# Kernel tuning notes

Measured on AMD Instinct MI355X. Metric: run time of the kernel, lower is better.

## Reference

```python
import jax, jax.numpy as jnp
import numpy as np

NEG_SLOPE = 0.2


def gat_conv(x, W, att_s, att_d, bias, src, dst, heads, out_c, concat):
    n = x.shape[0]
    h = (x @ W).reshape(n, heads, out_c)                      # [N,H,C]
    a_s = (h * att_s).sum(-1)                                 # [N,H]
    a_d = (h * att_d).sum(-1)                                 # [N,H]
    logits = jax.nn.leaky_relu(a_s[src] + a_d[dst], NEG_SLOPE)  # [E,H]
    # segment softmax over incoming edges of each dst node (per head)
    m = jax.ops.segment_max(logits, dst, num_segments=n)
    e = jnp.exp(logits - m[dst])
    denom = jax.ops.segment_sum(e, dst, num_segments=n)
    alpha = e / denom[dst]                                    # [E,H]
    msg = h[src] * alpha[:, :, None]                          # [E,H,C]
    out = jax.ops.segment_sum(msg, dst, num_segments=n)       # [N,H,C]
    out = out.reshape(n, heads * out_c) if concat else out.mean(axis=1)
    return out + bias


def setup_inputs() -> dict:
    key = jax.random.key(0)
    ks = jax.random.split(key, 9)
    N, IN, OUT, E = 100000, 256, 40, 1600000
    return {
        "x": jax.random.normal(ks[0], (N, IN), jnp.float32),
        "edge_index": jax.random.randint(ks[1], (2, E), 0, N, jnp.int32),
        "W1": jax.random.normal(ks[2], (IN, 64), jnp.float32) * (1.0 / np.sqrt(IN)),
        "att_src1": jax.random.normal(ks[3], (8, 8), jnp.float32) * 0.1,
        "att_dst1": jax.random.normal(ks[4], (8, 8), jnp.float32) * 0.1,
        "b1": jnp.zeros((64,), jnp.float32),
        "W2": jax.random.normal(ks[5], (64, OUT), jnp.float32) * (1.0 / 8.0),
        "att_src2": jax.random.normal(ks[6], (1, OUT), jnp.float32) * 0.1,
        "att_dst2": jax.random.normal(ks[7], (1, OUT), jnp.float32) * 0.1,
        "b2": jnp.zeros((OUT,), jnp.float32),
    }


def reference(x, edge_index, W1, att_src1, att_dst1, b1, W2, att_src2, att_dst2, b2):
    n = x.shape[0]
    loop = jnp.arange(n, dtype=edge_index.dtype)
    src = jnp.concatenate([edge_index[0], loop])  # self-loops (PyG default)
    dst = jnp.concatenate([edge_index[1], loop])
    h = gat_conv(x, W1, att_src1, att_dst1, b1, src, dst, heads=8, out_c=8, concat=True)
    h = jax.nn.relu(h)
    out = gat_conv(h, W2, att_src2, att_dst2, b2, src, dst, heads=1, out_c=W2.shape[1], concat=True)
    return jax.nn.log_softmax(out, axis=1)
```

## Files before the change

kernel.cpp:

```cpp
#include <hip/hip_runtime.h>


#define L_IN   256
#define L_C1   64
#define L_H1   8
#define L_OUT  40
#define BCAP   5120

typedef __attribute__((ext_vector_type(8))) short short8;
typedef __attribute__((ext_vector_type(4))) float f32x4;

__device__ __forceinline__ float leaky(float x){ return fmaxf(x, 0.2f*x); }
__device__ __forceinline__ unsigned f2bf(float f){
  unsigned u = __float_as_uint(f);
  return (u + 0x7fffu + ((u >> 16) & 1u)) >> 16;
}
__device__ __forceinline__ float bflo(unsigned u){ return __uint_as_float(u << 16); }
__device__ __forceinline__ float bfhi(unsigned u){ return __uint_as_float(u & 0xffff0000u); }

__global__ __launch_bounds__(256) void prep_w1(const float* __restrict__ W1,
                                               ushort* __restrict__ wt,
                                               int* __restrict__ gcur, int NB){
  const int t = threadIdx.x;
  if (blockIdx.x == 4){
    for (int i = t; i < NB; i += 256) gcur[i] = 0;
    return;
  }
  __shared__ float ws[64][65];
  const int kb = blockIdx.x;
  #pragma unroll
  for (int i = 0; i < 16; ++i){
    int idx = t + i*256;
    ws[idx >> 6][idx & 63] = W1[(size_t)(kb*64 + (idx >> 6))*64 + (idx & 63)];
  }
  __syncthreads();
  int c  = t >> 2;
  int j0 = (t & 3) * 16;
  ushort tmp[16];
  #pragma unroll
  for (int j = 0; j < 16; ++j) tmp[j] = (ushort)f2bf(ws[j0 + j][c]);
  uint4* dst = (uint4*)(wt + (size_t)c*256 + kb*64 + j0);
  dst[0] = *(uint4*)&tmp[0];
  dst[1] = *(uint4*)&tmp[8];
}

__global__ __launch_bounds__(256) void bin_scatter(const int* __restrict__ esrc,
    const int* __restrict__ edst, int* __restrict__ gcur,
    unsigned* __restrict__ binned, int E, int NB){
  __shared__ int hist[512], rbase[512], cur[512];
  const int t  = threadIdx.x;
  const int e0 = blockIdx.x * 4096;
  hist[t] = 0; hist[t+256] = 0; cur[t] = 0; cur[t+256] = 0;
  __syncthreads();
  int sv[16], dv[16];
  const bool full = (e0 + 4096 <= E);
  if (full){
    #pragma unroll
    for (int j = 0; j < 4; ++j){
      int p4 = (e0 >> 2) + j*256 + t;
      int4 s4 = ((const int4*)esrc)[p4];
      int4 d4 = ((const int4*)edst)[p4];
      sv[4*j+0]=s4.x; sv[4*j+1]=s4.y; sv[4*j+2]=s4.z; sv[4*j+3]=s4.w;
      dv[4*j+0]=d4.x; dv[4*j+1]=d4.y; dv[4*j+2]=d4.z; dv[4*j+3]=d4.w;
      atomicAdd(&hist[d4.x >> 8], 1); atomicAdd(&hist[d4.y >> 8], 1);
      atomicAdd(&hist[d4.z >> 8], 1); atomicAdd(&hist[d4.w >> 8], 1);
    }
  } else {
    #pragma unroll
    for (int j = 0; j < 16; ++j){
      int idx = e0 + j*256 + t;
      if (idx < E){
        sv[j] = esrc[idx]; dv[j] = edst[idx];
        atomicAdd(&hist[dv[j] >> 8], 1);
      } else dv[j] = -1;
    }
  }
  __syncthreads();
  if (hist[t])                   rbase[t]     = atomicAdd(&gcur[t],     hist[t]);
  if (t+256 < NB && hist[t+256]) rbase[t+256] = atomicAdd(&gcur[t+256], hist[t+256]);
  __syncthreads();
  #pragma unroll
  for (int j = 0; j < 16; ++j){
    if (dv[j] >= 0){
      int b = dv[j] >> 8;
      int off = rbase[b] + atomicAdd(&cur[b], 1);
      if (off < BCAP)
        binned[(size_t)b*BCAP + off] =
          (unsigned)sv[j] | ((unsigned)(dv[j] & 255) << 17);
    }
  }
}

__global__ __launch_bounds__(256) void csr_gemm1(
    const unsigned* __restrict__ binned, const int* __restrict__ gcur,
    int2* __restrict__ nodeptr, int* __restrict__ csr, int NBK,
    const float* __restrict__ x, const ushort* __restrict__ wt,
    const float* __restrict__ atts, const float* __restrict__ attd,
    ushort* __restrict__ h1b, float* __restrict__ as1, float* __restrict__ ad1,
    int n, int ntiles, int npb)
{
  __shared__ __align__(16) char smem[43008];
  const int t   = threadIdx.x;
  const int bid = blockIdx.x;

  if (bid < NBK){
    unsigned* ebuf = (unsigned*)smem;
    int* cnt  = (int*)(smem + BCAP*4);
    int* pref = cnt + 256;
    int* cur  = pref + 256;
    const int b = bid;
    int ne = gcur[b]; if (ne > BCAP) ne = BCAP;
    const int base = b * BCAP;
    cnt[t] = 0; cur[t] = 0;
    __syncthreads();
    for (int i = t; i < ne; i += 256){
      unsigned e = binned[base + i];
      ebuf[i] = e;
      atomicAdd(&cnt[(e >> 17) & 255u], 1);
    }
    __syncthreads();
    pref[t] = cnt[t];
    __syncthreads();
    for (int off = 1; off < 256; off <<= 1){
      int a = (t >= off) ? pref[t-off] : 0;
      __syncthreads();
      pref[t] += a;
      __syncthreads();
    }
    int excl = pref[t] - cnt[t];
    __syncthreads();
    pref[t] = excl;
    int d = (b << 8) + t;
    if (d < n) nodeptr[d] = make_int2(base + excl, cnt[t]);
    __syncthreads();
    for (int i = t; i < ne; i += 256){
      unsigned e = ebuf[i];
      int ln = (int)((e >> 17) & 255u);
      int pos = base + pref[ln] + atomicAdd(&cur[ln], 1);
      csr[pos] = (int)(e & 0x1FFFFu);
    }
    return;
  }

  ushort (*ws)[264] = (ushort(*)[264])(smem);
  ushort (*hs)[72]  = (ushort(*)[72]) (smem + 33792);
  const int wv = t >> 6;
  const int ln = t & 63;
  const int fr = ln & 15;
  const int fq = ln >> 4;

  #pragma unroll
  for (int i = 0; i < 8; ++i){
    int idx = t + i*256;
    int row = idx >> 5, c8 = idx & 31;
    *(uint4*)&ws[row][c8*8] = *(const uint4*)(wt + (size_t)row*256 + c8*8);
  }
  __syncthreads();

  for (int tile = bid - NBK; tile < ntiles; tile += npb){
    const int rb = tile * 64;
    const int ar = rb + wv*16 + fr;
    const bool rv = ar < n;
    const float* xr = x + (size_t)(rv ? ar : 0) * L_IN;

    f32x4 acc[4];
    #pragma unroll
    for (int cb = 0; cb < 4; ++cb) acc[cb] = (f32x4){0.f,0.f,0.f,0.f};

    #pragma unroll
    for (int kk = 0; kk < 8; ++kk){
      const int k0 = kk*32 + fq*8;
      float4 a0 = make_float4(0.f,0.f,0.f,0.f), a1 = a0;
      if (rv){
        a0 = *(const float4*)(xr + k0);
        a1 = *(const float4*)(xr + k0 + 4);
      }
      uint4 au;
      au.x = f2bf(a0.x) | (f2bf(a0.y) << 16);
      au.y = f2bf(a0.z) | (f2bf(a0.w) << 16);
      au.z = f2bf(a1.x) | (f2bf(a1.y) << 16);
      au.w = f2bf(a1.z) | (f2bf(a1.w) << 16);
      short8 a = *(short8*)&au;
      #pragma unroll
      for (int cb = 0; cb < 4; ++cb){
        short8 b = *(const short8*)&ws[cb*16 + fr][k0];
        acc[cb] = __builtin_amdgcn_mfma_f32_16x16x32_bf16(a, b, acc[cb], 0, 0, 0);
      }
    }

    #pragma unroll
    for (int cb = 0; cb < 4; ++cb)
      #pragma unroll
      for (int r = 0; r < 4; ++r)
        hs[wv*16 + fq*4 + r][cb*16 + fr] = (ushort)f2bf(acc[cb][r]);

    #pragma unroll
    for (int i = 0; i < 2; ++i){
      int task = ln + i*64;
      int lrow = task >> 3;
      int sub  = task & 7;
      int row  = rb + wv*16 + lrow;
      if (row < n){
        uint4 u = *(const uint4*)&hs[wv*16 + lrow][sub*8];
        *(uint4*)(h1b + (size_t)row*L_C1 + sub*8) = u;
        float v0=bflo(u.x), v1=bfhi(u.x), v2=bflo(u.y), v3=bfhi(u.y);
        float v4=bflo(u.z), v5=bfhi(u.z), v6=bflo(u.w), v7=bfhi(u.w);
        const float* sa = atts + sub*8;
        const float* da = attd + sub*8;
        float ds = v0*sa[0]+v1*sa[1]+v2*sa[2]+v3*sa[3]+v4*sa[4]+v5*sa[5]+v6*sa[6]+v7*sa[7];
        float dd = v0*da[0]+v1*da[1]+v2*da[2]+v3*da[3]+v4*da[4]+v5*da[5]+v6*da[6]+v7*da[7];
        as1[(size_t)row*L_H1 + sub] = ds;
        ad1[(size_t)row*L_H1 + sub] = dd;
      }
    }
  }
}

__global__ __launch_bounds__(256) void agg1_kernel(
    const int2* __restrict__ nodeptr, const int* __restrict__ csr,
    const ushort* __restrict__ h1b, const float* __restrict__ as1,
    const float* __restrict__ ad1, const float* __restrict__ b1,
    ushort* __restrict__ hrb, int n)
{
  int wid  = (blockIdx.x*blockDim.x + threadIdx.x) >> 6;
  int lane = threadIdx.x & 63;
  if (wid >= n) return;
  int2 np  = nodeptr[wid];
  int beg  = np.x;
  int degt = np.y + 1;

  const int h  = lane & 7;
  const int eg = lane >> 3;
  const int cq = lane & 15;
  const int eq = lane >> 4;
  const int hw = cq >> 1;

  float adn = ad1[(size_t)wid*L_H1 + h];
  float a0 = 0.f, a1 = 0.f, a2 = 0.f, a3 = 0.f, sp = 0.f;

  #define A1_GRP_W(g, SRCV, WV)                                            \
    { int i_ = (g)*8 + eg;                                                 \
      SRCV = (i_ < degt-1) ? csr[beg + i_] : wid;                          \
      float l_ = (i_ < degt) ? leaky(as1[(size_t)SRCV*L_H1 + h] + adn)     \
                             : -1e30f;                                     \
      WV = __expf(l_); sp += WV; }
  #define A1_GRP_G(SRCV, WV)                                               \
    _Pragma("unroll")                                                      \
    for (int e0 = 0; e0 < 8; e0 += 4){                                     \
      int e_  = e0 + eq;                                                   \
      float we_ = __shfl(WV,   e_*8 + hw);                                 \
      int   se_ = __shfl(SRCV, e_*8);                                      \
      uint2 u_ = *(const uint2*)(h1b + (size_t)se_*L_C1 + cq*4);           \
      a0 += we_ * bflo(u_.x);                                              \
      a1 += we_ * bfhi(u_.x);                                              \
      a2 += we_ * bflo(u_.y);                                              \
      a3 += we_ * bfhi(u_.y);                                              \
    }

  if (degt <= 16){
    int s0, s1; float w0, w1;
    A1_GRP_W(0, s0, w0) A1_GRP_W(1, s1, w1)
    A1_GRP_G(s0, w0) A1_GRP_G(s1, w1)
  } else if (degt <= 24){
    int s0, s1, s2; float w0, w1, w2;
    A1_GRP_W(0, s0, w0) A1_GRP_W(1, s1, w1) A1_GRP_W(2, s2, w2)
    A1_GRP_G(s0, w0) A1_GRP_G(s1, w1) A1_GRP_G(s2, w2)
  } else {
    const int ngrp = (degt + 7) >> 3;
    for (int g = 0; g < ngrp; ++g){
      int sg; float wg;
      A1_GRP_W(g, sg, wg)
      A1_GRP_G(sg, wg)
    }
  }
  #undef A1_GRP_W
  #undef A1_GRP_G

  #pragma unroll
  for (int off = 8; off < 64; off <<= 1) sp += __shfl_xor(sp, off);
  float rinv = 1.0f / __shfl(sp, hw);
  a0 += __shfl_xor(a0, 16); a0 += __shfl_xor(a0, 32);
  a1 += __shfl_xor(a1, 16); a1 += __shfl_xor(a1, 32);
  a2 += __shfl_xor(a2, 16); a2 += __shfl_xor(a2, 32);
  a3 += __shfl_xor(a3, 16); a3 += __shfl_xor(a3, 32);
  if (lane < 16){
    float4 bv = *(const float4*)&b1[cq*4];
    float r0 = fmaxf(a0*rinv + bv.x, 0.f);
    float r1 = fmaxf(a1*rinv + bv.y, 0.f);
    float r2 = fmaxf(a2*rinv + bv.z, 0.f);
    float r3 = fmaxf(a3*rinv + bv.w, 0.f);
    uint2 o;
    o.x = f2bf(r0) | (f2bf(r1) << 16);
    o.y = f2bf(r2) | (f2bf(r3) << 16);
    *(uint2*)(hrb + (size_t)wid*L_C1 + cq*4) = o;
  }
}

__global__ __launch_bounds__(256) void gemm2_kernel(
    const ushort* __restrict__ hrb, const float* __restrict__ W2,
    const float* __restrict__ atts2, const float* __restrict__ attd2,
    ushort* __restrict__ h2b, float* __restrict__ as2, float* __restrict__ ad2, int n)
{
  __shared__ float w2s[64*40];
  const int t = threadIdx.x;
  for (int i = t; i < 64*40; i += 256) w2s[i] = W2[i];
  __syncthreads();
  int row = blockIdx.x*256 + t;
  if (row >= n) return;

  uint4 rv[8];
  #pragma unroll
  for (int q = 0; q < 8; ++q)
    rv[q] = *(const uint4*)(hrb + (size_t)row*L_C1 + q*8);

  f32x4 acc4[10];
  #pragma unroll
  for (int j = 0; j < 10; ++j) acc4[j] = (f32x4){0.f,0.f,0.f,0.f};

  #pragma unroll
  for (int q = 0; q < 8; ++q){
    unsigned uu[4] = {rv[q].x, rv[q].y, rv[q].z, rv[q].w};
    #pragma unroll
    for (int d = 0; d < 4; ++d){
      int k = q*8 + d*2;
      float v0 = bflo(uu[d]), v1 = bfhi(uu[d]);
      const f32x4* w0 = (const f32x4*)&w2s[k*40];
      const f32x4* w1 = (const f32x4*)&w2s[(k+1)*40];
      #pragma unroll
      for (int j = 0; j < 10; ++j) acc4[j] += v0*w0[j] + v1*w1[j];
    }
  }

  float acc[40];
  #pragma unroll
  for (int j = 0; j < 10; ++j){
    acc[4*j+0]=acc4[j][0]; acc[4*j+1]=acc4[j][1];
    acc[4*j+2]=acc4[j][2]; acc[4*j+3]=acc4[j][3];
  }
  float ps = 0.f, pd = 0.f;
  #pragma unroll
  for (int j = 0; j < 40; ++j){ ps += acc[j]*atts2[j]; pd += acc[j]*attd2[j]; }
  unsigned pk[20];
  #pragma unroll
  for (int q = 0; q < 20; ++q) pk[q] = f2bf(acc[2*q]) | (f2bf(acc[2*q+1]) << 16);
  uint4* dst = (uint4*)(h2b + (size_t)row*L_OUT);
  #pragma unroll
  for (int q = 0; q < 5; ++q) dst[q] = make_uint4(pk[4*q],pk[4*q+1],pk[4*q+2],pk[4*q+3]);
  as2[row] = ps;
  ad2[row] = pd;
}

__global__ __launch_bounds__(256) void agg2_kernel(
    const int2* __restrict__ nodeptr, const int* __restrict__ csr,
    const ushort* __restrict__ h2b, const float* __restrict__ as2,
    const float* __restrict__ ad2, const float* __restrict__ b2,
    float* __restrict__ out, int n)
{
  int wid  = (blockIdx.x*blockDim.x + threadIdx.x) >> 6;
  int lane = threadIdx.x & 63;
  if (wid >= n) return;
  int2 np  = nodeptr[wid];
  int beg  = np.x;
  int degt = np.y + 1;

  const int eidx = (lane < 60) ? (lane / 20) : 0;
  const int cq   = (lane < 60) ? (lane % 20) : 0;

  float adn = ad2[wid];
  float ax = 0.f, ay = 0.f, sp = 0.f;

  #define A2_STEP(e_, SRCV, WV, CNT)                                       \
    { int ee_ = (e_);                                                      \
      int es_ = (ee_ < 64) ? ee_ : 63;                                     \
      float we_ = __shfl(WV,   es_);                                       \
      int   se_ = __shfl(SRCV, es_);                                       \
      we_ = (ee_ < (CNT)) ? we_ : 0.f;                                     \
      unsigned u_ = *(const unsigned*)(h2b + (size_t)se_*L_OUT + cq*2);    \
      ax += we_ * bflo(u_);                                                \
      ay += we_ * bfhi(u_); }

  if (degt <= 64){
    int i = lane;
    int src = (i < degt-1) ? csr[beg + i] : wid;
    float l = (i < degt) ? leaky(as2[src] + adn) : -1e30f;
    float w = __expf(l);
    sp = w;
    if (degt <= 18){
      #pragma unroll
      for (int j = 0; j < 2; ++j){
        A2_STEP(j*9 + 0*3 + eidx, src, w, degt)
        A2_STEP(j*9 + 1*3 + eidx, src, w, degt)
        A2_STEP(j*9 + 2*3 + eidx, src, w, degt)
      }
    } else if (degt <= 27){
      #pragma unroll
      for (int j = 0; j < 3; ++j){
        A2_STEP(j*9 + 0*3 + eidx, src, w, degt)
        A2_STEP(j*9 + 1*3 + eidx, src, w, degt)
        A2_STEP(j*9 + 2*3 + eidx, src, w, degt)
      }
    } else if (degt <= 36){
      #pragma unroll
      for (int j = 0; j < 4; ++j){
        A2_STEP(j*9 + 0*3 + eidx, src, w, degt)
        A2_STEP(j*9 + 1*3 + eidx, src, w, degt)
        A2_STEP(j*9 + 2*3 + eidx, src, w, degt)
      }
    } else {
      for (int e0 = 0; e0 < degt; e0 += 9){
        A2_STEP(e0 + 0*3 + eidx, src, w, degt)
        A2_STEP(e0 + 1*3 + eidx, src, w, degt)
        A2_STEP(e0 + 2*3 + eidx, src, w, degt)
      }
    }
  } else {
    const int ngrp = (degt + 63) >> 6;
    for (int g = 0; g < ngrp; ++g){
      int i = g*64 + lane;
      int src = (i < degt-1) ? csr[beg + i] : wid;
      float l = (i < degt) ? leaky(as2[src] + adn) : -1e30f;
      float w = __expf(l);
      sp += w;
      int cnt = degt - g*64; if (cnt > 64) cnt = 64;
      for (int e0 = 0; e0 < cnt; e0 += 9){
        A2_STEP(e0 + 0*3 + eidx, src, w, cnt)
        A2_STEP(e0 + 1*3 + eidx, src, w, cnt)
        A2_STEP(e0 + 2*3 + eidx, src, w, cnt)
      }
    }
  }
  #undef A2_STEP

  #pragma unroll
  for (int off = 1; off < 64; off <<= 1) sp += __shfl_xor(sp, off);
  float rinv = 1.0f / sp;

  float ax0 = __shfl(ax, cq), ax1 = __shfl(ax, cq+20), ax2 = __shfl(ax, cq+40);
  float ay0 = __shfl(ay, cq), ay1 = __shfl(ay, cq+20), ay2 = __shfl(ay, cq+40);
  float axs = (ax0 + ax1) + ax2;
  float ays = (ay0 + ay1) + ay2;

  bool act = (lane < 20);
  float o0 = axs*rinv + b2[cq*2];
  float o1 = ays*rinv + b2[cq*2+1];
  float mx = act ? fmaxf(o0, o1) : -1e30f;
  #pragma unroll
  for (int off = 1; off < 32; off <<= 1) mx = fmaxf(mx, __shfl_xor(mx, off));
  float ex = act ? (__expf(o0 - mx) + __expf(o1 - mx)) : 0.f;
  #pragma unroll
  for (int off = 1; off < 32; off <<= 1) ex += __shfl_xor(ex, off);
  float lse = mx + __logf(ex);
  if (act){
    float2 r = make_float2(o0 - lse, o1 - lse);
    *(float2*)(out + (size_t)wid*L_OUT + cq*2) = r;
  }
}

extern "C" void kernel_launch(void* const* d_in, const int* in_sizes, int n_in,
                              void* d_out, int out_size, void* d_ws, size_t ws_size,
                              hipStream_t stream)
{
  const float* x    = (const float*)d_in[0];
  const int*   ei   = (const int*)  d_in[1];
  const float* W1   = (const float*)d_in[2];
  const float* as1w = (const float*)d_in[3];
  const float* ad1w = (const float*)d_in[4];
  const float* b1   = (const float*)d_in[5];
  const float* W2   = (const float*)d_in[6];
  const float* as2w = (const float*)d_in[7];
  const float* ad2w = (const float*)d_in[8];
  const float* b2   = (const float*)d_in[9];

  const int N = in_sizes[0] / L_IN;
  const int E = in_sizes[1] / 2;
  const int NB = (N + 255) >> 8;
  const int NSC = (E + 4095) / 4096;
  const int NT1 = (N + 63) / 64;
  const int NPB = (NT1 < 768) ? NT1 : 768;
  const int* esrc = ei;
  const int* edst = ei + E;
  float* out = (float*)d_out;

  char* w = (char*)d_ws;
  auto alloc = [&](size_t bytes)->char*{
    char* p = w; w += (bytes + 255) & ~size_t(255); return p;
  };
  ushort* h1b  = (ushort*)alloc((size_t)N*L_C1*2);
  float*  as1  = (float*) alloc((size_t)N*L_H1*4);
  float*  ad1  = (float*) alloc((size_t)N*L_H1*4);
  size_t union_sz = (size_t)N*L_C1*2 + (size_t)N*L_OUT*2;
  if (union_sz < (size_t)NB*BCAP*4) union_sz = (size_t)NB*BCAP*4;
  char*  ub    = alloc(union_sz);
  ushort* hrb  = (ushort*)ub;
  ushort* h2b  = (ushort*)(ub + (size_t)N*L_C1*2);
  unsigned* binned = (unsigned*)ub;
  float*  as2  = (float*) alloc((size_t)N*4);
  float*  ad2  = (float*) alloc((size_t)N*4);
  ushort* wt   = (ushort*)alloc((size_t)64*256*2);
  int2*  nodeptr=(int2*)  alloc((size_t)N*8);
  int*   csr   = (int*)   alloc((size_t)NB*BCAP*4);
  int*   gcur  = (int*)   alloc((size_t)NB*4);

  prep_w1     <<<5,          256, 0, stream>>>(W1, wt, gcur, NB);
  bin_scatter <<<NSC,        256, 0, stream>>>(esrc, edst, gcur, binned, E, NB);
  csr_gemm1   <<<NB + NPB,   256, 0, stream>>>(binned, gcur, nodeptr, csr, NB,
                                               x, wt, as1w, ad1w, h1b, as1, ad1,
                                               N, NT1, NPB);
  agg1_kernel <<<(N+3)/4,    256, 0, stream>>>(nodeptr, csr, h1b, as1, ad1, b1, hrb, N);
  gemm2_kernel<<<(N+255)/256,256, 0, stream>>>(hrb, W2, as2w, ad2w, h2b, as2, ad2, N);
  agg2_kernel <<<(N+3)/4,    256, 0, stream>>>(nodeptr, csr, h2b, as2, ad2, b2, out, N);
}
```

Before: 175.5 us.

## Restructure GAT aggregation lanes: edge-per-lane-group with 16B row gathers, pad h2 rows

Both aggregation kernels now give each group of 8 lanes one edge: each lane loads a full 16-byte chunk of the source row and accumulates 8 channels, with no per-edge weight and source shuffles. The h2 buffer is padded to a 64-element row stride so the layer-2 gathers are 16-byte aligned. Cross-edge reduction becomes one xor-shuffle tree over 8 accumulators. This removes shuffle traffic and narrow 4-8 byte gathers. In exchange it costs extra h2 storage, more registers per lane, and idle lanes (3 of 8) in layer 2.

```diff
diff --git a/kernel.cpp b/kernel.cpp
--- a/kernel.cpp
+++ b/kernel.cpp
@@ -5,6 +5,7 @@
 #define L_C1   64
 #define L_H1   8
 #define L_OUT  40
+#define H2S    64
 #define BCAP   5120
 
 typedef __attribute__((ext_vector_type(8))) short short8;
@@ -231,75 +232,71 @@
 
   const int h  = lane & 7;
   const int eg = lane >> 3;
-  const int cq = lane & 15;
-  const int eq = lane >> 4;
-  const int hw = cq >> 1;
 
   float adn = ad1[(size_t)wid*L_H1 + h];
-  float a0 = 0.f, a1 = 0.f, a2 = 0.f, a3 = 0.f, sp = 0.f;
-
-  #define A1_GRP_W(g, SRCV, WV)                                            \
+  float a0=0.f,a1=0.f,a2=0.f,a3=0.f,a4=0.f,a5=0.f,a6=0.f,a7=0.f,sp=0.f;
+
+  #define A1_W(g, SRCV, WV)                                                \
     { int i_ = (g)*8 + eg;                                                 \
       SRCV = (i_ < degt-1) ? csr[beg + i_] : wid;                          \
       float l_ = (i_ < degt) ? leaky(as1[(size_t)SRCV*L_H1 + h] + adn)     \
                              : -1e30f;                                     \
       WV = __expf(l_); sp += WV; }
-  #define A1_GRP_G(SRCV, WV)                                               \
-    _Pragma("unroll")                                                      \
-    for (int e0 = 0; e0 < 8; e0 += 4){                                     \
-      int e_  = e0 + eq;                                                   \
-      float we_ = __shfl(WV,   e_*8 + hw);                                 \
-      int   se_ = __shfl(SRCV, e_*8);                                      \
-      uint2 u_ = *(const uint2*)(h1b + (size_t)se_*L_C1 + cq*4);           \
-      a0 += we_ * bflo(u_.x);                                              \
-      a1 += we_ * bfhi(u_.x);                                              \
-      a2 += we_ * bflo(u_.y);                                              \
-      a3 += we_ * bfhi(u_.y);                                              \
-    }
+  #define A1_G(SRCV, WV)                                                   \
+    { uint4 u_ = *(const uint4*)(h1b + (size_t)SRCV*L_C1 + h*8);           \
+      a0 += WV*bflo(u_.x); a1 += WV*bfhi(u_.x);                            \
+      a2 += WV*bflo(u_.y); a3 += WV*bfhi(u_.y);                            \
+      a4 += WV*bflo(u_.z); a5 += WV*bfhi(u_.z);                            \
+      a6 += WV*bflo(u_.w); a7 += WV*bfhi(u_.w); }
 
   if (degt <= 16){
     int s0, s1; float w0, w1;
-    A1_GRP_W(0, s0, w0) A1_GRP_W(1, s1, w1)
-    A1_GRP_G(s0, w0) A1_GRP_G(s1, w1)
+    A1_W(0, s0, w0) A1_W(1, s1, w1)
+    A1_G(s0, w0) A1_G(s1, w1)
   } else if (degt <= 24){
     int s0, s1, s2; float w0, w1, w2;
-    A1_GRP_W(0, s0, w0) A1_GRP_W(1, s1, w1) A1_GRP_W(2, s2, w2)
-    A1_GRP_G(s0, w0) A1_GRP_G(s1, w1) A1_GRP_G(s2, w2)
+    A1_W(0, s0, w0) A1_W(1, s1, w1) A1_W(2, s2, w2)
+    A1_G(s0, w0) A1_G(s1, w1) A1_G(s2, w2)
   } else {
     const int ngrp = (degt + 7) >> 3;
     for (int g = 0; g < ngrp; ++g){
       int sg; float wg;
-      A1_GRP_W(g, sg, wg)
-      A1_GRP_G(sg, wg)
-    }
-  }
-  #undef A1_GRP_W
-  #undef A1_GRP_G
-
-  #pragma unroll
-  for (int off = 8; off < 64; off <<= 1) sp += __shfl_xor(sp, off);
-  float rinv = 1.0f / __shfl(sp, hw);
-  a0 += __shfl_xor(a0, 16); a0 += __shfl_xor(a0, 32);
-  a1 += __shfl_xor(a1, 16); a1 += __shfl_xor(a1, 32);
-  a2 += __shfl_xor(a2, 16); a2 += __shfl_xor(a2, 32);
-  a3 += __shfl_xor(a3, 16); a3 += __shfl_xor(a3, 32);
-  if (lane < 16){
-    float4 bv = *(const float4*)&b1[cq*4];
-    float r0 = fmaxf(a0*rinv + bv.x, 0.f);
-    float r1 = fmaxf(a1*rinv + bv.y, 0.f);
-    float r2 = fmaxf(a2*rinv + bv.z, 0.f);
-    float r3 = fmaxf(a3*rinv + bv.w, 0.f);
-    uint2 o;
+      A1_W(g, sg, wg)
+      A1_G(sg, wg)
+    }
+  }
+  #undef A1_W
+  #undef A1_G
+
+  #pragma unroll
+  for (int off = 8; off < 64; off <<= 1){
+    sp += __shfl_xor(sp, off);
+    a0 += __shfl_xor(a0, off); a1 += __shfl_xor(a1, off);
+    a2 += __shfl_xor(a2, off); a3 += __shfl_xor(a3, off);
+    a4 += __shfl_xor(a4, off); a5 += __shfl_xor(a5, off);
+    a6 += __shfl_xor(a6, off); a7 += __shfl_xor(a7, off);
+  }
+  float rinv = 1.0f / sp;
+  if (lane < 8){
+    float4 bA = *(const float4*)&b1[h*8];
+    float4 bB = *(const float4*)&b1[h*8 + 4];
+    float r0 = fmaxf(a0*rinv + bA.x, 0.f), r1 = fmaxf(a1*rinv + bA.y, 0.f);
+    float r2 = fmaxf(a2*rinv + bA.z, 0.f), r3 = fmaxf(a3*rinv + bA.w, 0.f);
+    float r4 = fmaxf(a4*rinv + bB.x, 0.f), r5 = fmaxf(a5*rinv + bB.y, 0.f);
+    float r6 = fmaxf(a6*rinv + bB.z, 0.f), r7 = fmaxf(a7*rinv + bB.w, 0.f);
+    uint4 o;
     o.x = f2bf(r0) | (f2bf(r1) << 16);
     o.y = f2bf(r2) | (f2bf(r3) << 16);
-    *(uint2*)(hrb + (size_t)wid*L_C1 + cq*4) = o;
+    o.z = f2bf(r4) | (f2bf(r5) << 16);
+    o.w = f2bf(r6) | (f2bf(r7) << 16);
+    *(uint4*)(hrb + (size_t)wid*L_C1 + h*8) = o;
   }
 }
 
 __global__ __launch_bounds__(256) void gemm2_kernel(
     const ushort* __restrict__ hrb, const float* __restrict__ W2,
     const float* __restrict__ atts2, const float* __restrict__ attd2,
-    ushort* __restrict__ h2b, float* __restrict__ as2, float* __restrict__ ad2, int n)
+    ushort* __restrict__ h2p, float* __restrict__ as2, float* __restrict__ ad2, int n)
 {
   __shared__ float w2s[64*40];
   const int t = threadIdx.x;
@@ -343,7 +340,7 @@
   unsigned pk[20];
   #pragma unroll
   for (int q = 0; q < 20; ++q) pk[q] = f2bf(acc[2*q]) | (f2bf(acc[2*q+1]) << 16);
-  uint4* dst = (uint4*)(h2b + (size_t)row*L_OUT);
+  uint4* dst = (uint4*)(h2p + (size_t)row*H2S);
   #pragma unroll
   for (int q = 0; q < 5; ++q) dst[q] = make_uint4(pk[4*q],pk[4*q+1],pk[4*q+2],pk[4*q+3]);
   as2[row] = ps;
@@ -352,7 +349,7 @@
 
 __global__ __launch_bounds__(256) void agg2_kernel(
     const int2* __restrict__ nodeptr, const int* __restrict__ csr,
-    const ushort* __restrict__ h2b, const float* __restrict__ as2,
+    const ushort* __restrict__ h2p, const float* __restrict__ as2,
     const float* __restrict__ ad2, const float* __restrict__ b2,
     float* __restrict__ out, int n)
 {
@@ -363,96 +360,81 @@
   int beg  = np.x;
   int degt = np.y + 1;
 
-  const int eidx = (lane < 60) ? (lane / 20) : 0;
-  const int cq   = (lane < 60) ? (lane % 20) : 0;
+  const int o  = lane & 7;
+  const int eg = lane >> 3;
 
   float adn = ad2[wid];
-  float ax = 0.f, ay = 0.f, sp = 0.f;
-
-  #define A2_STEP(e_, SRCV, WV, CNT)                                       \
-    { int ee_ = (e_);                                                      \
-      int es_ = (ee_ < 64) ? ee_ : 63;                                     \
-      float we_ = __shfl(WV,   es_);                                       \
-      int   se_ = __shfl(SRCV, es_);                                       \
-      we_ = (ee_ < (CNT)) ? we_ : 0.f;                                     \
-      unsigned u_ = *(const unsigned*)(h2b + (size_t)se_*L_OUT + cq*2);    \
-      ax += we_ * bflo(u_);                                                \
-      ay += we_ * bfhi(u_); }
-
-  if (degt <= 64){
-    int i = lane;
-    int src = (i < degt-1) ? csr[beg + i] : wid;
-    float l = (i < degt) ? leaky(as2[src] + adn) : -1e30f;
-    float w = __expf(l);
-    sp = w;
-    if (degt <= 18){
-      #pragma unroll
-      for (int j = 0; j < 2; ++j){
-        A2_STEP(j*9 + 0*3 + eidx, src, w, degt)
-        A2_STEP(j*9 + 1*3 + eidx, src, w, degt)
-        A2_STEP(j*9 + 2*3 + eidx, src, w, degt)
-      }
-    } else if (degt <= 27){
-      #pragma unroll
-      for (int j = 0; j < 3; ++j){
-        A2_STEP(j*9 + 0*3 + eidx, src, w, degt)
-        A2_STEP(j*9 + 1*3 + eidx, src, w, degt)
-        A2_STEP(j*9 + 2*3 + eidx, src, w, degt)
-      }
-    } else if (degt <= 36){
-      #pragma unroll
-      for (int j = 0; j < 4; ++j){
-        A2_STEP(j*9 + 0*3 + eidx, src, w, degt)
-        A2_STEP(j*9 + 1*3 + eidx, src, w, degt)
-        A2_STEP(j*9 + 2*3 + eidx, src, w, degt)
-      }
-    } else {
-      for (int e0 = 0; e0 < degt; e0 += 9){
-        A2_STEP(e0 + 0*3 + eidx, src, w, degt)
-        A2_STEP(e0 + 1*3 + eidx, src, w, degt)
-        A2_STEP(e0 + 2*3 + eidx, src, w, degt)
-      }
-    }
+  float a0=0.f,a1=0.f,a2=0.f,a3=0.f,a4=0.f,a5=0.f,a6=0.f,a7=0.f,sp=0.f;
+
+  #define A2_W(g, SRCV, WV)                                                \
+    { int i_ = (g)*8 + eg;                                                 \
+      SRCV = (i_ < degt-1) ? csr[beg + i_] : wid;                          \
+      float l_ = (i_ < degt) ? leaky(as2[SRCV] + adn) : -1e30f;            \
+      WV = __expf(l_); sp += WV; }
+  #define A2_G(SRCV, WV)                                                   \
+    { uint4 u_ = *(const uint4*)(h2p + (size_t)SRCV*H2S + o*8);            \
+      a0 += WV*bflo(u_.x); a1 += WV*bfhi(u_.x);                            \
+      a2 += WV*bflo(u_.y); a3 += WV*bfhi(u_.y);                            \
+      a4 += WV*bflo(u_.z); a5 += WV*bfhi(u_.z);                            \
+      a6 += WV*bflo(u_.w); a7 += WV*bfhi(u_.w); }
+
+  if (degt <= 16){
+    int s0, s1; float w0, w1;
+    A2_W(0, s0, w0) A2_W(1, s1, w1)
+    A2_G(s0, w0) A2_G(s1, w1)
+  } else if (degt <= 24){
+    int s0, s1, s2; float w0, w1, w2;
+    A2_W(0, s0, w0) A2_W(1, s1, w1) A2_W(2, s2, w2)
+    A2_G(s0, w0) A2_G(s1, w1) A2_G(s2, w2)
+  } else if (degt <= 32){
+    int s0, s1, s2, s3; float w0, w1, w2, w3;
+    A2_W(0, s0, w0) A2_W(1, s1, w1) A2_W(2, s2, w2) A2_W(3, s3, w3)
+    A2_G(s0, w0) A2_G(s1, w1) A2_G(s2, w2) A2_G(s3, w3)
   } else {
-    const int ngrp = (degt + 63) >> 6;
+    const int ngrp = (degt + 7) >> 3;
     for (int g = 0; g < ngrp; ++g){
-      int i = g*64 + lane;
-      int src = (i < degt-1) ? csr[beg + i] : wid;
-      float l = (i < degt) ? leaky(as2[src] + adn) : -1e30f;
-      float w = __expf(l);
-      sp += w;
-      int cnt = degt - g*64; if (cnt > 64) cnt = 64;
-      for (int e0 = 0; e0 < cnt; e0 += 9){
-        A2_STEP(e0 + 0*3 + eidx, src, w, cnt)
-        A2_STEP(e0 + 1*3 + eidx, src, w, cnt)
-        A2_STEP(e0 + 2*3 + eidx, src, w, cnt)
-      }
-    }
-  }
-  #undef A2_STEP
-
-  #pragma unroll
-  for (int off = 1; off < 64; off <<= 1) sp += __shfl_xor(sp, off);
+      int sg; float wg;
+      A2_W(g, sg, wg)
+      A2_G(sg, wg)
+    }
+  }
+  #undef A2_W
+  #undef A2_G
+
+  #pragma unroll
+  for (int off = 8; off < 64; off <<= 1){
+    sp += __shfl_xor(sp, off);
+    a0 += __shfl_xor(a0, off); a1 += __shfl_xor(a1, off);
+    a2 += __shfl_xor(a2, off); a3 += __shfl_xor(a3, off);
+    a4 += __shfl_xor(a4, off); a5 += __shfl_xor(a5, off);
+    a6 += __shfl_xor(a6, off); a7 += __shfl_xor(a7, off);
+  }
   float rinv = 1.0f / sp;
 
-  float ax0 = __shfl(ax, cq), ax1 = __shfl(ax, cq+20), ax2 = __shfl(ax, cq+40);
-  float ay0 = __shfl(ay, cq), ay1 = __shfl(ay, cq+20), ay2 = __shfl(ay, cq+40);
-  float axs = (ax0 + ax1) + ax2;
-  float ays = (ay0 + ay1) + ay2;
-
-  bool act = (lane < 20);
-  float o0 = axs*rinv + b2[cq*2];
-  float o1 = ays*rinv + b2[cq*2+1];
-  float mx = act ? fmaxf(o0, o1) : -1e30f;
-  #pragma unroll
-  for (int off = 1; off < 32; off <<= 1) mx = fmaxf(mx, __shfl_xor(mx, off));
-  float ex = act ? (__expf(o0 - mx) + __expf(o1 - mx)) : 0.f;
-  #pragma unroll
-  for (int off = 1; off < 32; off <<= 1) ex += __shfl_xor(ex, off);
+  const bool act = (o < 5);
+  const int  bo  = (act ? o : 0) * 8;
+  float4 bA = *(const float4*)&b2[bo];
+  float4 bB = *(const float4*)&b2[bo + 4];
+  float c0 = a0*rinv + bA.x, c1 = a1*rinv + bA.y;
+  float c2 = a2*rinv + bA.z, c3 = a3*rinv + bA.w;
+  float c4 = a4*rinv + bB.x, c5 = a5*rinv + bB.y;
+  float c6 = a6*rinv + bB.z, c7 = a7*rinv + bB.w;
+
+  float mx = act ? fmaxf(fmaxf(fmaxf(c0,c1),fmaxf(c2,c3)),
+                         fmaxf(fmaxf(c4,c5),fmaxf(c6,c7))) : -1e30f;
+  #pragma unroll
+  for (int off = 1; off < 8; off <<= 1) mx = fmaxf(mx, __shfl_xor(mx, off));
+  float ex = act ? (__expf(c0-mx)+__expf(c1-mx)+__expf(c2-mx)+__expf(c3-mx)
+                   +__expf(c4-mx)+__expf(c5-mx)+__expf(c6-mx)+__expf(c7-mx)) : 0.f;
+  #pragma unroll
+  for (int off = 1; off < 8; off <<= 1) ex += __shfl_xor(ex, off);
   float lse = mx + __logf(ex);
-  if (act){
-    float2 r = make_float2(o0 - lse, o1 - lse);
-    *(float2*)(out + (size_t)wid*L_OUT + cq*2) = r;
+  if (lane < 5){
+    float4 rA = make_float4(c0-lse, c1-lse, c2-lse, c3-lse);
+    float4 rB = make_float4(c4-lse, c5-lse, c6-lse, c7-lse);
+    float* op = out + (size_t)wid*L_OUT + o*8;
+    *(float4*)op = rA;
+    *(float4*)(op+4) = rB;
   }
 }
 
@@ -488,11 +470,11 @@
   ushort* h1b  = (ushort*)alloc((size_t)N*L_C1*2);
   float*  as1  = (float*) alloc((size_t)N*L_H1*4);
   float*  ad1  = (float*) alloc((size_t)N*L_H1*4);
-  size_t union_sz = (size_t)N*L_C1*2 + (size_t)N*L_OUT*2;
+  size_t union_sz = (size_t)N*L_C1*2 + (size_t)N*H2S*2;
   if (union_sz < (size_t)NB*BCAP*4) union_sz = (size_t)NB*BCAP*4;
   char*  ub    = alloc(union_sz);
   ushort* hrb  = (ushort*)ub;
-  ushort* h2b  = (ushort*)(ub + (size_t)N*L_C1*2);
+  ushort* h2p  = (ushort*)(ub + (size_t)N*L_C1*2);
   unsigned* binned = (unsigned*)ub;
   float*  as2  = (float*) alloc((size_t)N*4);
   float*  ad2  = (float*) alloc((size_t)N*4);
@@ -507,6 +489,6 @@
                                                x, wt, as1w, ad1w, h1b, as1, ad1,
                                                N, NT1, NPB);
   agg1_kernel <<<(N+3)/4,    256, 0, stream>>>(nodeptr, csr, h1b, as1, ad1, b1, hrb, N);
-  gemm2_kernel<<<(N+255)/256,256, 0, stream>>>(hrb, W2, as2w, ad2w, h2b, as2, ad2, N);
-  agg2_kernel <<<(N+3)/4,    256, 0, stream>>>(nodeptr, csr, h2b, as2, ad2, b2, out, N);
-}
+  gemm2_kernel<<<(N+255)/256,256, 0, stream>>>(hrb, W2, as2w, ad2w, h2p, as2, ad2, N);
+  agg2_kernel <<<(N+3)/4,    256, 0, stream>>>(nodeptr, csr, h2p, as2, ad2, b2, out, N);
+}
```

Result: slower. 183.3 us (+4.4%).
